# Performance work log

Hardware: AMD Instinct MI355X
Metric: run time of the kernel (lower is better)

Reference implementation:

```python
import jax, jax.numpy as jnp
import numpy as np

WH = WW = 7
SHIFT = 3
H = W = 56
NUM_HEADS = 8
DIM = 256
NW = (H // WH) * (W // WW)  # 64 windows per image
B = 64  # images


def _make_coords_table():
    rch = np.arange(-(WH - 1), WH, dtype=np.float32)
    rcw = np.arange(-(WW - 1), WW, dtype=np.float32)
    t = np.stack(np.meshgrid(rch, rcw, indexing='ij'), axis=-1)[None]  # (1,13,13,2)
    t[..., 0] /= (WH - 1)
    t[..., 1] /= (WW - 1)
    t *= 8.0
    t = np.sign(t) * np.log2(np.abs(t) + 1.0) / np.log2(8.0)
    return t.astype(np.float32)


def _make_rel_pos_index():
    coords = np.stack(np.meshgrid(np.arange(WH), np.arange(WW), indexing='ij'))  # (2,Wh,Ww)
    cf = coords.reshape(2, -1)
    rel = (cf[:, :, None] - cf[:, None, :]).transpose(1, 2, 0)  # (N,N,2)
    rel[..., 0] += WH - 1
    rel[..., 1] += WW - 1
    rel[..., 0] *= 2 * WW - 1
    return rel.sum(-1).astype(np.int32)  # (49,49)


def _make_shift_mask():
    img = np.zeros((H, W), dtype=np.float32)
    cnt = 0
    for hs in (slice(0, -WH), slice(-WH, -SHIFT), slice(-SHIFT, None)):
        for ws in (slice(0, -WW), slice(-WW, -SHIFT), slice(-SHIFT, None)):
            img[hs, ws] = cnt
            cnt += 1
    win = img.reshape(H // WH, WH, W // WW, WW).transpose(0, 2, 1, 3).reshape(-1, WH * WW)
    diff = win[:, None, :] - win[:, :, None]
    return np.where(diff != 0, -100.0, 0.0).astype(np.float32)  # (nW,49,49)


def setup_inputs() -> dict:
    key = jax.random.key(0)
    ks = jax.random.split(key, 10)
    N = WH * WW
    B_ = B * NW
    s = 0.02
    return {
        'x': jax.random.normal(ks[0], (B_, N, DIM), jnp.float32),
        'qkv_w': jax.random.normal(ks[1], (3 * DIM, DIM), jnp.float32) * s,
        'q_bias': jax.random.normal(ks[2], (DIM,), jnp.float32) * s,
        'v_bias': jax.random.normal(ks[3], (DIM,), jnp.float32) * s,
        'logit_scale': jnp.full((NUM_HEADS, 1, 1), np.log(10.0), jnp.float32),
        'cpb_w1': jax.random.normal(ks[4], (512, 2), jnp.float32) * 0.5,
        'cpb_b1': jax.random.normal(ks[5], (512,), jnp.float32) * s,
        'cpb_w2': jax.random.normal(ks[6], (NUM_HEADS, 512), jnp.float32) * 0.05,
        'relative_coords_table': jnp.asarray(_make_coords_table()),
        'relative_position_index': jnp.asarray(_make_rel_pos_index()),
        'attn_mask': jnp.asarray(_make_shift_mask()),
        'proj_w': jax.random.normal(ks[7], (DIM, DIM), jnp.float32) * s,
        'proj_b': jax.random.normal(ks[8], (DIM,), jnp.float32) * s,
    }


def reference(x, qkv_w, q_bias, v_bias, logit_scale, cpb_w1, cpb_b1, cpb_w2,
              relative_coords_table, relative_position_index, attn_mask,
              proj_w, proj_b):
    B_, N, C = x.shape
    nH = logit_scale.shape[0]
    hd = C // nH
    nW = attn_mask.shape[0]
    # qkv projection; k has no bias (SwinV2)
    qkv_bias = jnp.concatenate([q_bias, jnp.zeros_like(v_bias), v_bias])
    qkv = x @ qkv_w.T + qkv_bias
    qkv = qkv.reshape(B_, N, 3, nH, hd).transpose(2, 0, 3, 1, 4)  # (3,B_,nH,N,hd)
    q, k, v = qkv[0], qkv[1], qkv[2]
    # cosine attention (eps matches fused kernel)
    eps = 1e-6
    qn = q * jax.lax.rsqrt(jnp.sum(q * q, axis=-1, keepdims=True) + eps)
    kn = k * jax.lax.rsqrt(jnp.sum(k * k, axis=-1, keepdims=True) + eps)
    attn = jnp.einsum('bhnd,bhmd->bhnm', qn, kn)
    scale = jnp.exp(jnp.minimum(logit_scale, jnp.log(100.0)))  # (nH,1,1), clamp max
    attn = attn * scale[None]
    # continuous relative position bias via CPB MLP
    hcpb = jax.nn.relu(relative_coords_table @ cpb_w1.T + cpb_b1)  # (1,13,13,512)
    table = (hcpb @ cpb_w2.T).reshape(-1, nH)  # (169,nH)
    rpb = table[relative_position_index.reshape(-1)].reshape(N, N, nH).transpose(2, 0, 1)
    rpb = 16.0 * jax.nn.sigmoid(rpb)  # (nH,N,N)
    attn = attn + rpb[None]
    # shift-window mask
    attn = attn.reshape(B_ // nW, nW, nH, N, N) + attn_mask[None, :, None]
    attn = attn.reshape(B_, nH, N, N)
    attn = jax.nn.softmax(attn, axis=-1)
    out = jnp.einsum('bhnm,bhmd->bhnd', attn, v)
    out = out.transpose(0, 2, 1, 3).reshape(B_, N, C)
    return out @ proj_w.T + proj_b
```

## Files before the change

kernel.cpp:

```cpp
#include <hip/hip_runtime.h>
#include <stdint.h>

typedef unsigned short u16;
typedef unsigned int u32;
typedef __attribute__((ext_vector_type(8))) short s16x8;
typedef __attribute__((ext_vector_type(4))) float f32x4;

__device__ __forceinline__ u16 f2bf(float f) {
  union { float f; u32 u; } v; v.f = f;
  u32 u = v.u;
  return (u16)((u + 0x7fffu + ((u >> 16) & 1u)) >> 16);
}
__device__ __forceinline__ float bf2f_lo(u32 u) {
  union { u32 uu; float f; } v; v.uu = u << 16; return v.f;
}
__device__ __forceinline__ float bf2f_hi(u32 u) {
  union { u32 uu; float f; } v; v.uu = u & 0xffff0000u; return v.f;
}
__device__ __forceinline__ void cvt8(uint4 w, float* f) {
  f[0] = bf2f_lo(w.x); f[1] = bf2f_hi(w.x);
  f[2] = bf2f_lo(w.y); f[3] = bf2f_hi(w.y);
  f[4] = bf2f_lo(w.z); f[5] = bf2f_hi(w.z);
  f[6] = bf2f_lo(w.w); f[7] = bf2f_hi(w.w);
}

#define NT 49
#define CD 256
#define NWIN 4096
#define SB_RS 520
#define SX_RS 264
#define SVT_RS 72

#define L_SX  0
#define L_SB  33792
#define L_SVT 100352
#define L_SRQ 137216
#define L_SRK 139264
#define L_TOTAL 141312

#define WS_BIASC 8192
#define WS_WQKV  (8192 + 524288)
#define WS_WPROJ (532480 + 393216)

__global__ void cpb_table_kernel(const float* __restrict__ coords,
                                 const float* __restrict__ w1,
                                 const float* __restrict__ b1,
                                 const float* __restrict__ w2,
                                 float* __restrict__ table) {
  int t = blockIdx.x * 256 + threadIdx.x;
  if (t >= 169 * 8) return;
  int p = t >> 3, h = t & 7;
  float c0 = coords[p * 2], c1 = coords[p * 2 + 1];
  float acc = 0.f;
  for (int j = 0; j < 512; ++j) {
    float hid = fmaf(c0, w1[j * 2], fmaf(c1, w1[j * 2 + 1], b1[j]));
    hid = fmaxf(hid, 0.f);
    acc = fmaf(hid, w2[h * 512 + j], acc);
  }
  table[t] = acc;
}

__global__ void biasc_prep(const float* __restrict__ table,
                           const int* __restrict__ rpi,
                           const float* __restrict__ mask,
                           float* __restrict__ biasC) {
  int idx = blockIdx.x * 256 + threadIdx.x;
  if (idx >= 4 * 8 * 4096) return;
  int t = idx >> 15;
  int h = (idx >> 12) & 7;
  int q = (idx >> 6) & 63;
  int kv = idx & 63;
  float v = -1e9f;
  if (q < 49 && kv < 49) {
    float tb = table[rpi[q * 49 + kv] * 8 + h];
    float rpb = 16.f / (1.f + __expf(-tb));
    int wimg = ((t & 2) ? 56 : 0) + ((t & 1) ? 7 : 0);
    v = rpb + mask[wimg * 2401 + q * 49 + kv];
  }
  biasC[idx] = v;
}

__global__ void wcvt_kernel(const float* __restrict__ qkv_w,
                            const float* __restrict__ proj_w,
                            u16* __restrict__ wq, u16* __restrict__ wp) {
  int t = blockIdx.x * 256 + threadIdx.x;
  if (t >= 32768) return;
  const float* src; u16* dst; int idx;
  if (t < 24576) { idx = t; src = qkv_w; dst = wq + (size_t)idx * 8; }
  else           { idx = t - 24576; src = proj_w; dst = wp + (size_t)idx * 8; }
  int nt = idx >> 9, rem = idx & 511;
  int kk = rem >> 6, l = rem & 63;
  int n = nt * 16 + (l & 15);
  int k = kk * 32 + (l >> 4) * 8;
  const float4* s = (const float4*)(src + (size_t)n * 256 + k);
  float4 v0 = s[0], v1 = s[1];
  u32 w0 = (u32)f2bf(v0.x) | ((u32)f2bf(v0.y) << 16);
  u32 w1 = (u32)f2bf(v0.z) | ((u32)f2bf(v0.w) << 16);
  u32 w2 = (u32)f2bf(v1.x) | ((u32)f2bf(v1.y) << 16);
  u32 w3 = (u32)f2bf(v1.z) | ((u32)f2bf(v1.w) << 16);
  *(uint4*)dst = make_uint4(w0, w1, w2, w3);
}

template<int V0>
__device__ __forceinline__ void p2_body(
    const u16* sX, u16* sB, u16* sVT, const u16* wqb,
    const float* __restrict__ q_bias, const float* __restrict__ v_bias,
    const int hh, const int lr, const int lg) {
  f32x4 acc[6][4];
#pragma unroll
  for (int nt = 0; nt < 6; ++nt)
#pragma unroll
    for (int mt = 0; mt < 4; ++mt) acc[nt][mt] = (f32x4){0.f, 0.f, 0.f, 0.f};
  s16x8 bcur[6], bnxt[6];
#pragma unroll
  for (int nt = 0; nt < 6; ++nt)
    bcur[nt] = *(const s16x8*)&wqb[(nt * 8 + 0) * 512];
#pragma unroll
  for (int kk = 0; kk < 8; ++kk) {
    if (kk < 7) {
#pragma unroll
      for (int nt = 0; nt < 6; ++nt)
        bnxt[nt] = *(const s16x8*)&wqb[(nt * 8 + kk + 1) * 512];
    }
    s16x8 a[4];
#pragma unroll
    for (int mt = 0; mt < 4; ++mt)
      a[mt] = *(const s16x8*)&sX[(mt * 16 + lr) * SX_RS + kk * 32 + lg * 8];
#pragma unroll
    for (int nt = 0; nt < 6; ++nt)
#pragma unroll
      for (int mt = 0; mt < 4; ++mt)
        acc[nt][mt] = (nt < V0)
            ? __builtin_amdgcn_mfma_f32_16x16x32_bf16(bcur[nt], a[mt], acc[nt][mt], 0, 0, 0)
            : __builtin_amdgcn_mfma_f32_16x16x32_bf16(a[mt], bcur[nt], acc[nt][mt], 0, 0, 0);
#pragma unroll
    for (int nt = 0; nt < 6; ++nt) bcur[nt] = bnxt[nt];
  }
#pragma unroll
  for (int nt = 0; nt < 6; ++nt) {
    const int n0 = hh * 96 + nt * 16;
    if (nt < V0) {
      const int r = n0 >> 8;
      const int cb = (n0 & 255) + 4 * lg;
      float4 bq = make_float4(0.f, 0.f, 0.f, 0.f);
      if (r == 0) bq = *(const float4*)(q_bias + cb);
      const int coff = (r << 8) + cb;
#pragma unroll
      for (int mt = 0; mt < 4; ++mt) {
        const int token = mt * 16 + lr;
        if (token < NT) {
          uint2 pk;
          pk.x = (u32)f2bf(acc[nt][mt][0] + bq.x) | ((u32)f2bf(acc[nt][mt][1] + bq.y) << 16);
          pk.y = (u32)f2bf(acc[nt][mt][2] + bq.z) | ((u32)f2bf(acc[nt][mt][3] + bq.w) << 16);
          *(uint2*)&sB[token * SB_RS + coff] = pk;
        }
      }
    } else {
      const int c0 = (n0 & 255) + lr;
      const float bv = v_bias[c0];
      u16* vtb = &sVT[c0 * SVT_RS];
#pragma unroll
      for (int mt = 0; mt < 4; ++mt) {
        const int row0 = mt * 16 + lg * 4;
        float v0 = acc[nt][mt][0] + bv, v1 = acc[nt][mt][1] + bv;
        float v2 = acc[nt][mt][2] + bv, v3 = acc[nt][mt][3] + bv;
        if (mt < 3) {
          uint2 pk2;
          pk2.x = (u32)f2bf(v0) | ((u32)f2bf(v1) << 16);
          pk2.y = (u32)f2bf(v2) | ((u32)f2bf(v3) << 16);
          *(uint2*)&vtb[row0] = pk2;
        } else {
          if (row0     < NT) vtb[row0]     = f2bf(v0);
          if (row0 + 1 < NT) vtb[row0 + 1] = f2bf(v1);
          if (row0 + 2 < NT) vtb[row0 + 2] = f2bf(v2);
          if (row0 + 3 < NT) vtb[row0 + 3] = f2bf(v3);
        }
      }
    }
  }
}

__global__ __launch_bounds__(512, 2) void swin_fused(
    const float* __restrict__ x,
    const float* __restrict__ q_bias, const float* __restrict__ v_bias,
    const float* __restrict__ logit_scale, const float* __restrict__ biasC,
    const u16* __restrict__ wq, const u16* __restrict__ wp,
    const float* __restrict__ proj_b,
    float* __restrict__ out) {
  __shared__ __attribute__((aligned(16))) unsigned char smem[L_TOTAL];
  u16*   sX  = (u16*)(smem + L_SX);
  u16*   sB  = (u16*)(smem + L_SB);
  u16*   sVT = (u16*)(smem + L_SVT);
  float* sRQ = (float*)(smem + L_SRQ);
  float* sRK = (float*)(smem + L_SRK);

  const int tid = threadIdx.x;
  const int wid = blockIdx.x;
  const int wimg = wid & 63;
  const int hh = tid >> 6;
  const int il = tid & 63;
  const int lr = il & 15;
  const int lg = il >> 4;

  float4 xr[6]; float4 xr6;
  {
    const float4* xg = (const float4*)(x + (size_t)wid * (NT * CD));
#pragma unroll
    for (int i = 0; i < 6; ++i) xr[i] = xg[tid + 512 * i];
    if (tid < 64) xr6 = xg[3072 + tid];
  }
  const float scl = __expf(fminf(logit_scale[hh], 4.605170186f));
  {
    u32* zx = (u32*)&sX[49 * SX_RS];
    for (int e = tid; e < 1980; e += 512) zx[e] = 0;
    u32* zb = (u32*)&sB[49 * SB_RS];
    for (int e = tid; e < 3900; e += 512) zb[e] = 0;
    u32* zv = (u32*)sVT;
    for (int e = tid; e < 9216; e += 512) zv[e] = 0;
  }
  {
#pragma unroll
    for (int i = 0; i < 6; ++i) {
      const int e = tid + 512 * i;
      const int row = e >> 6, c4 = e & 63;
      float4 v = xr[i];
      u32 w0 = (u32)f2bf(v.x) | ((u32)f2bf(v.y) << 16);
      u32 w1 = (u32)f2bf(v.z) | ((u32)f2bf(v.w) << 16);
      *(uint2*)&sX[row * SX_RS + c4 * 4] = make_uint2(w0, w1);
    }
    if (tid < 64) {
      const int e = 3072 + tid;
      const int row = e >> 6, c4 = e & 63;
      float4 v = xr6;
      u32 w0 = (u32)f2bf(v.x) | ((u32)f2bf(v.y) << 16);
      u32 w1 = (u32)f2bf(v.z) | ((u32)f2bf(v.w) << 16);
      *(uint2*)&sX[row * SX_RS + c4 * 4] = make_uint2(w0, w1);
    }
  }
  __syncthreads();

  {
    const u16* wqb = wq + (size_t)hh * 24576 + il * 8;
    if (hh < 5)       p2_body<6>(sX, sB, sVT, wqb, q_bias, v_bias, hh, lr, lg);
    else if (hh == 5) p2_body<2>(sX, sB, sVT, wqb, q_bias, v_bias, hh, lr, lg);
    else              p2_body<0>(sX, sB, sVT, wqb, q_bias, v_bias, hh, lr, lg);
  }
  __syncthreads();

  {
    float rqs = 0.f, rkv = 0.f;
    if (il < NT) {
      const uint4* qb4 = (const uint4*)&sB[il * SB_RS + hh * 32];
      const uint4* kb4 = (const uint4*)&sB[il * SB_RS + 256 + hh * 32];
      const int rot = (il >> 3) & 3;
      float f[8];
      float sq = 1e-6f, sk = 1e-6f;
#pragma unroll
      for (int c = 0; c < 4; ++c) {
        const int cg = (c + rot) & 3;
        cvt8(qb4[cg], f);
#pragma unroll
        for (int j = 0; j < 8; ++j) sq = fmaf(f[j], f[j], sq);
      }
#pragma unroll
      for (int c = 0; c < 4; ++c) {
        const int cg = (c + rot) & 3;
        cvt8(kb4[cg], f);
#pragma unroll
        for (int j = 0; j < 8; ++j) sk = fmaf(f[j], f[j], sk);
      }
      rqs = rsqrtf(sq) * scl;
      rkv = rsqrtf(sk);
    }
    sRQ[hh * 64 + il] = rqs;
    sRK[hh * 64 + il] = rkv;
    asm volatile("s_waitcnt lgkmcnt(0)" ::: "memory");
    __builtin_amdgcn_sched_barrier(0);
  }

  {
    const int h = hh;
    const int type = (((wimg >> 3) == 7) ? 2 : 0) | (((wimg & 7) == 7) ? 1 : 0);
    const float* bp = biasC + ((size_t)(type * 8 + h) << 12);
    f32x4 bias[4][4];
#pragma unroll
    for (int nt = 0; nt < 4; ++nt)
#pragma unroll
      for (int mt = 0; mt < 4; ++mt)
        bias[nt][mt] = *(const f32x4*)(bp + (lr + 16 * nt) * 64 + 16 * mt + 4 * lg);
    s16x8 ka[4], qb[4];
#pragma unroll
    for (int mt = 0; mt < 4; ++mt)
      ka[mt] = *(const s16x8*)&sB[(lr + 16 * mt) * SB_RS + 256 + h * 32 + lg * 8];
#pragma unroll
    for (int nt = 0; nt < 4; ++nt)
      qb[nt] = *(const s16x8*)&sB[(lr + 16 * nt) * SB_RS + h * 32 + lg * 8];
    f32x4 sacc[4][4];
#pragma unroll
    for (int nt = 0; nt < 4; ++nt)
#pragma unroll
      for (int mt = 0; mt < 4; ++mt)
        sacc[nt][mt] = __builtin_amdgcn_mfma_f32_16x16x32_bf16(
            ka[mt], qb[nt], (f32x4){0.f, 0.f, 0.f, 0.f}, 0, 0, 0);
    f32x4 rk4[4];
#pragma unroll
    for (int mt = 0; mt < 4; ++mt)
      rk4[mt] = *(const f32x4*)&sRK[h * 64 + 16 * mt + 4 * lg];
    float invv[4];
#pragma unroll
    for (int nt = 0; nt < 4; ++nt) {
      const float rq_ = sRQ[h * 64 + lr + 16 * nt];
      float mx = -3e38f;
#pragma unroll
      for (int mt = 0; mt < 4; ++mt)
#pragma unroll
        for (int i = 0; i < 4; ++i) {
          float tv = fmaf(sacc[nt][mt][i] * rk4[mt][i], rq_, bias[nt][mt][i]);
          sacc[nt][mt][i] = tv;
          mx = fmaxf(mx, tv);
        }
      mx = fmaxf(mx, __shfl_xor(mx, 16, 64));
      mx = fmaxf(mx, __shfl_xor(mx, 32, 64));
      float sm = 0.f;
#pragma unroll
      for (int mt = 0; mt < 4; ++mt)
#pragma unroll
        for (int i = 0; i < 4; ++i) {
          float e = __expf(sacc[nt][mt][i] - mx);
          sacc[nt][mt][i] = e;
          sm += e;
        }
      sm += __shfl_xor(sm, 16, 64);
      sm += __shfl_xor(sm, 32, 64);
      invv[nt] = 1.0f / sm;
    }
    u32 pkk[4][4][2];
#pragma unroll
    for (int nt = 0; nt < 4; ++nt)
#pragma unroll
      for (int mt = 0; mt < 4; ++mt) {
        pkk[nt][mt][0] = (u32)f2bf(sacc[nt][mt][0]) | ((u32)f2bf(sacc[nt][mt][1]) << 16);
        pkk[nt][mt][1] = (u32)f2bf(sacc[nt][mt][2]) | ((u32)f2bf(sacc[nt][mt][3]) << 16);
      }
    s16x8 vb[2][2];
#pragma unroll
    for (int nd = 0; nd < 2; ++nd)
#pragma unroll
      for (int s = 0; s < 2; ++s)
        vb[nd][s] = *(const s16x8*)&sVT[(h * 32 + nd * 16 + lr) * SVT_RS + lg * 8 + 32 * s];
    const int srcA = lr + ((il & 16) << 1);
    const int srcB = srcA + 16;
    const bool gh = (il & 32) != 0;
    f32x4 oacc[4][2];
#pragma unroll
    for (int mo = 0; mo < 4; ++mo)
#pragma unroll
      for (int nd = 0; nd < 2; ++nd) oacc[mo][nd] = (f32x4){0.f, 0.f, 0.f, 0.f};
#pragma unroll
    for (int mo = 0; mo < 4; ++mo) {
#pragma unroll
      for (int s = 0; s < 2; ++s) {
        u32 a0 = (u32)__shfl((int)pkk[mo][2 * s][0],     srcA, 64);
        u32 b0 = (u32)__shfl((int)pkk[mo][2 * s + 1][0], srcA, 64);
        u32 a1 = (u32)__shfl((int)pkk[mo][2 * s][1],     srcA, 64);
        u32 b1 = (u32)__shfl((int)pkk[mo][2 * s + 1][1], srcA, 64);
        u32 a2 = (u32)__shfl((int)pkk[mo][2 * s][0],     srcB, 64);
        u32 b2 = (u32)__shfl((int)pkk[mo][2 * s + 1][0], srcB, 64);
        u32 a3 = (u32)__shfl((int)pkk[mo][2 * s][1],     srcB, 64);
        u32 b3 = (u32)__shfl((int)pkk[mo][2 * s + 1][1], srcB, 64);
        union { u32 u[4]; s16x8 v; } pu;
        pu.u[0] = gh ? b0 : a0;
        pu.u[1] = gh ? b1 : a1;
        pu.u[2] = gh ? b2 : a2;
        pu.u[3] = gh ? b3 : a3;
#pragma unroll
        for (int nd = 0; nd < 2; ++nd)
          oacc[mo][nd] = __builtin_amdgcn_mfma_f32_16x16x32_bf16(
              vb[nd][s], pu.v, oacc[mo][nd], 0, 0, 0);
      }
    }
#pragma unroll
    for (int mo = 0; mo < 4; ++mo) {
      const int q = 16 * mo + lr;
      if (q < NT) {
        const float invq = invv[mo];
#pragma unroll
        for (int nd = 0; nd < 2; ++nd) {
          uint2 pk;
          pk.x = (u32)f2bf(oacc[mo][nd][0] * invq) | ((u32)f2bf(oacc[mo][nd][1] * invq) << 16);
          pk.y = (u32)f2bf(oacc[mo][nd][2] * invq) | ((u32)f2bf(oacc[mo][nd][3] * invq) << 16);
          *(uint2*)&sX[q * SX_RS + h * 32 + nd * 16 + 4 * lg] = pk;
        }
      }
    }
  }
  s16x8 wpr[2][8];
  {
    const u16* wpb = wp + (size_t)hh * 8192 + il * 8;
#pragma unroll
    for (int nt = 0; nt < 2; ++nt)
#pragma unroll
      for (int kk = 0; kk < 8; ++kk)
        wpr[nt][kk] = *(const s16x8*)&wpb[(nt * 8 + kk) * 512];
  }
  float4 pb4[2];
#pragma unroll
  for (int nt = 0; nt < 2; ++nt)
    pb4[nt] = *(const float4*)(proj_b + hh * 32 + nt * 16 + 4 * lg);
  __syncthreads();

  {
    f32x4 acc[2][4];
#pragma unroll
    for (int nt = 0; nt < 2; ++nt)
#pragma unroll
      for (int mt = 0; mt < 4; ++mt) acc[nt][mt] = (f32x4){0.f, 0.f, 0.f, 0.f};
#pragma unroll
    for (int kk = 0; kk < 8; ++kk) {
      s16x8 a[4];
#pragma unroll
      for (int mt = 0; mt < 4; ++mt)
        a[mt] = *(const s16x8*)&sX[(mt * 16 + lr) * SX_RS + kk * 32 + lg * 8];
#pragma unroll
      for (int nt = 0; nt < 2; ++nt)
#pragma unroll
        for (int mt = 0; mt < 4; ++mt)
          acc[nt][mt] = __builtin_amdgcn_mfma_f32_16x16x32_bf16(
              wpr[nt][kk], a[mt], acc[nt][mt], 0, 0, 0);
    }
    float* og = out + (size_t)wid * (NT * CD);
#pragma unroll
    for (int mt = 0; mt < 4; ++mt) {
      const int token = mt * 16 + lr;
      if (token < NT) {
#pragma unroll
        for (int nt = 0; nt < 2; ++nt) {
          float4 st;
          st.x = acc[nt][mt][0] + pb4[nt].x;
          st.y = acc[nt][mt][1] + pb4[nt].y;
          st.z = acc[nt][mt][2] + pb4[nt].z;
          st.w = acc[nt][mt][3] + pb4[nt].w;
          *(float4*)&og[token * CD + hh * 32 + nt * 16 + 4 * lg] = st;
        }
      }
    }
  }
}

extern "C" void kernel_launch(void* const* d_in, const int* in_sizes, int n_in,
                              void* d_out, int out_size, void* d_ws, size_t ws_size,
                              hipStream_t stream) {
  (void)in_sizes; (void)n_in; (void)out_size; (void)ws_size;
  const float* x           = (const float*)d_in[0];
  const float* qkv_w       = (const float*)d_in[1];
  const float* q_bias      = (const float*)d_in[2];
  const float* v_bias      = (const float*)d_in[3];
  const float* logit_scale = (const float*)d_in[4];
  const float* cpb_w1      = (const float*)d_in[5];
  const float* cpb_b1      = (const float*)d_in[6];
  const float* cpb_w2      = (const float*)d_in[7];
  const float* coords      = (const float*)d_in[8];
  const int*   rpi         = (const int*)d_in[9];
  const float* mask        = (const float*)d_in[10];
  const float* proj_w      = (const float*)d_in[11];
  const float* proj_b      = (const float*)d_in[12];
  float* out = (float*)d_out;

  float* table = (float*)d_ws;
  float* biasC = (float*)((char*)d_ws + WS_BIASC);
  u16*   wq    = (u16*)((char*)d_ws + WS_WQKV);
  u16*   wp    = (u16*)((char*)d_ws + WS_WPROJ);

  hipLaunchKernelGGL(cpb_table_kernel, dim3(6), dim3(256), 0, stream,
                     coords, cpb_w1, cpb_b1, cpb_w2, table);
  hipLaunchKernelGGL(biasc_prep, dim3((4 * 8 * 4096 + 255) / 256), dim3(256),
                     0, stream, table, rpi, mask, biasC);
  hipLaunchKernelGGL(wcvt_kernel, dim3(128), dim3(256), 0, stream,
                     qkv_w, proj_w, wq, wp);
  hipLaunchKernelGGL(swin_fused, dim3(NWIN), dim3(512), 0, stream,
                     x, q_bias, v_bias, logit_scale, biasC,
                     wq, wp, proj_b, out);
}
```

Before: 634.7 us.

## Keep per-head Q/K/V in registers, shrink LDS, raise occupancy

Each wave now computes its own head's Q, K and V projections and keeps them in registers. Q/K normalization is done with cross-lane shuffles, and the data is reshaped into MFMA operand layout with shuffles instead of going through shared-memory staging buffers. LDS drops from about 141KB to only the X/output tile, and the launch bound requests 4 blocks per CU instead of 2. The CPB table kernel is also parallelized per position with a wave reduction. The main risk is register pressure at the higher occupancy target and repeated reads of X from LDS across the three projection passes.

```diff
diff --git a/kernel.cpp b/kernel.cpp
--- a/kernel.cpp
+++ b/kernel.cpp
@@ -11,32 +11,14 @@
   u32 u = v.u;
   return (u16)((u + 0x7fffu + ((u >> 16) & 1u)) >> 16);
 }
-__device__ __forceinline__ float bf2f_lo(u32 u) {
-  union { u32 uu; float f; } v; v.uu = u << 16; return v.f;
-}
-__device__ __forceinline__ float bf2f_hi(u32 u) {
-  union { u32 uu; float f; } v; v.uu = u & 0xffff0000u; return v.f;
-}
-__device__ __forceinline__ void cvt8(uint4 w, float* f) {
-  f[0] = bf2f_lo(w.x); f[1] = bf2f_hi(w.x);
-  f[2] = bf2f_lo(w.y); f[3] = bf2f_hi(w.y);
-  f[4] = bf2f_lo(w.z); f[5] = bf2f_hi(w.z);
-  f[6] = bf2f_lo(w.w); f[7] = bf2f_hi(w.w);
+__device__ __forceinline__ u32 pk2bf(float a, float b) {
+  return (u32)f2bf(a) | ((u32)f2bf(b) << 16);
 }
 
 #define NT 49
 #define CD 256
 #define NWIN 4096
-#define SB_RS 520
 #define SX_RS 264
-#define SVT_RS 72
-
-#define L_SX  0
-#define L_SB  33792
-#define L_SVT 100352
-#define L_SRQ 137216
-#define L_SRK 139264
-#define L_TOTAL 141312
 
 #define WS_BIASC 8192
 #define WS_WQKV  (8192 + 524288)
@@ -47,17 +29,29 @@
                                  const float* __restrict__ b1,
                                  const float* __restrict__ w2,
                                  float* __restrict__ table) {
-  int t = blockIdx.x * 256 + threadIdx.x;
-  if (t >= 169 * 8) return;
-  int p = t >> 3, h = t & 7;
-  float c0 = coords[p * 2], c1 = coords[p * 2 + 1];
-  float acc = 0.f;
-  for (int j = 0; j < 512; ++j) {
-    float hid = fmaf(c0, w1[j * 2], fmaf(c1, w1[j * 2 + 1], b1[j]));
-    hid = fmaxf(hid, 0.f);
-    acc = fmaf(hid, w2[h * 512 + j], acc);
-  }
-  table[t] = acc;
+  __shared__ float red[4][8];
+  const int p = blockIdx.x;
+  const int tid = threadIdx.x;
+  const float c0 = coords[p * 2], c1 = coords[p * 2 + 1];
+  float acc[8];
+#pragma unroll
+  for (int h = 0; h < 8; ++h) acc[h] = 0.f;
+  for (int j = tid; j < 512; j += 256) {
+    float hid = fmaxf(fmaf(c0, w1[j * 2], fmaf(c1, w1[j * 2 + 1], b1[j])), 0.f);
+#pragma unroll
+    for (int h = 0; h < 8; ++h) acc[h] = fmaf(hid, w2[h * 512 + j], acc[h]);
+  }
+#pragma unroll
+  for (int h = 0; h < 8; ++h) {
+    float v = acc[h];
+    v += __shfl_xor(v, 1, 64);  v += __shfl_xor(v, 2, 64);
+    v += __shfl_xor(v, 4, 64);  v += __shfl_xor(v, 8, 64);
+    v += __shfl_xor(v, 16, 64); v += __shfl_xor(v, 32, 64);
+    if ((tid & 63) == 0) red[tid >> 6][h] = v;
+  }
+  __syncthreads();
+  if (tid < 8)
+    table[p * 8 + tid] = red[0][tid] + red[1][tid] + red[2][tid] + red[3][tid];
 }
 
 __global__ void biasc_prep(const float* __restrict__ table,
@@ -94,105 +88,31 @@
   int k = kk * 32 + (l >> 4) * 8;
   const float4* s = (const float4*)(src + (size_t)n * 256 + k);
   float4 v0 = s[0], v1 = s[1];
-  u32 w0 = (u32)f2bf(v0.x) | ((u32)f2bf(v0.y) << 16);
-  u32 w1 = (u32)f2bf(v0.z) | ((u32)f2bf(v0.w) << 16);
-  u32 w2 = (u32)f2bf(v1.x) | ((u32)f2bf(v1.y) << 16);
-  u32 w3 = (u32)f2bf(v1.z) | ((u32)f2bf(v1.w) << 16);
-  *(uint4*)dst = make_uint4(w0, w1, w2, w3);
-}
-
-template<int V0>
-__device__ __forceinline__ void p2_body(
-    const u16* sX, u16* sB, u16* sVT, const u16* wqb,
-    const float* __restrict__ q_bias, const float* __restrict__ v_bias,
-    const int hh, const int lr, const int lg) {
-  f32x4 acc[6][4];
-#pragma unroll
-  for (int nt = 0; nt < 6; ++nt)
-#pragma unroll
-    for (int mt = 0; mt < 4; ++mt) acc[nt][mt] = (f32x4){0.f, 0.f, 0.f, 0.f};
-  s16x8 bcur[6], bnxt[6];
-#pragma unroll
-  for (int nt = 0; nt < 6; ++nt)
-    bcur[nt] = *(const s16x8*)&wqb[(nt * 8 + 0) * 512];
-#pragma unroll
-  for (int kk = 0; kk < 8; ++kk) {
-    if (kk < 7) {
-#pragma unroll
-      for (int nt = 0; nt < 6; ++nt)
-        bnxt[nt] = *(const s16x8*)&wqb[(nt * 8 + kk + 1) * 512];
-    }
-    s16x8 a[4];
-#pragma unroll
-    for (int mt = 0; mt < 4; ++mt)
-      a[mt] = *(const s16x8*)&sX[(mt * 16 + lr) * SX_RS + kk * 32 + lg * 8];
-#pragma unroll
-    for (int nt = 0; nt < 6; ++nt)
-#pragma unroll
-      for (int mt = 0; mt < 4; ++mt)
-        acc[nt][mt] = (nt < V0)
-            ? __builtin_amdgcn_mfma_f32_16x16x32_bf16(bcur[nt], a[mt], acc[nt][mt], 0, 0, 0)
-            : __builtin_amdgcn_mfma_f32_16x16x32_bf16(a[mt], bcur[nt], acc[nt][mt], 0, 0, 0);
-#pragma unroll
-    for (int nt = 0; nt < 6; ++nt) bcur[nt] = bnxt[nt];
-  }
-#pragma unroll
-  for (int nt = 0; nt < 6; ++nt) {
-    const int n0 = hh * 96 + nt * 16;
-    if (nt < V0) {
-      const int r = n0 >> 8;
-      const int cb = (n0 & 255) + 4 * lg;
-      float4 bq = make_float4(0.f, 0.f, 0.f, 0.f);
-      if (r == 0) bq = *(const float4*)(q_bias + cb);
-      const int coff = (r << 8) + cb;
-#pragma unroll
-      for (int mt = 0; mt < 4; ++mt) {
-        const int token = mt * 16 + lr;
-        if (token < NT) {
-          uint2 pk;
-          pk.x = (u32)f2bf(acc[nt][mt][0] + bq.x) | ((u32)f2bf(acc[nt][mt][1] + bq.y) << 16);
-          pk.y = (u32)f2bf(acc[nt][mt][2] + bq.z) | ((u32)f2bf(acc[nt][mt][3] + bq.w) << 16);
-          *(uint2*)&sB[token * SB_RS + coff] = pk;
-        }
-      }
-    } else {
-      const int c0 = (n0 & 255) + lr;
-      const float bv = v_bias[c0];
-      u16* vtb = &sVT[c0 * SVT_RS];
-#pragma unroll
-      for (int mt = 0; mt < 4; ++mt) {
-        const int row0 = mt * 16 + lg * 4;
-        float v0 = acc[nt][mt][0] + bv, v1 = acc[nt][mt][1] + bv;
-        float v2 = acc[nt][mt][2] + bv, v3 = acc[nt][mt][3] + bv;
-        if (mt < 3) {
-          uint2 pk2;
-          pk2.x = (u32)f2bf(v0) | ((u32)f2bf(v1) << 16);
-          pk2.y = (u32)f2bf(v2) | ((u32)f2bf(v3) << 16);
-          *(uint2*)&vtb[row0] = pk2;
-        } else {
-          if (row0     < NT) vtb[row0]     = f2bf(v0);
-          if (row0 + 1 < NT) vtb[row0 + 1] = f2bf(v1);
-          if (row0 + 2 < NT) vtb[row0 + 2] = f2bf(v2);
-          if (row0 + 3 < NT) vtb[row0 + 3] = f2bf(v3);
-        }
-      }
-    }
-  }
-}
-
-__global__ __launch_bounds__(512, 2) void swin_fused(
+  *(uint4*)dst = make_uint4(pk2bf(v0.x, v0.y), pk2bf(v0.z, v0.w),
+                            pk2bf(v1.x, v1.y), pk2bf(v1.z, v1.w));
+}
+
+__device__ __forceinline__ s16x8 gather4(const u32 lo0, const u32 lo1,
+                                         const u32 hi0, const u32 hi1,
+                                         int srcL, int srcH, bool hi) {
+  union { u32 u[4]; s16x8 v; } r;
+  u32 a0 = (u32)__shfl((int)lo0, srcL, 64), b0 = (u32)__shfl((int)hi0, srcL, 64);
+  u32 a1 = (u32)__shfl((int)lo1, srcL, 64), b1 = (u32)__shfl((int)hi1, srcL, 64);
+  u32 a2 = (u32)__shfl((int)lo0, srcH, 64), b2 = (u32)__shfl((int)hi0, srcH, 64);
+  u32 a3 = (u32)__shfl((int)lo1, srcH, 64), b3 = (u32)__shfl((int)hi1, srcH, 64);
+  r.u[0] = hi ? b0 : a0; r.u[1] = hi ? b1 : a1;
+  r.u[2] = hi ? b2 : a2; r.u[3] = hi ? b3 : a3;
+  return r.v;
+}
+
+__global__ __launch_bounds__(512, 4) void swin_fused(
     const float* __restrict__ x,
     const float* __restrict__ q_bias, const float* __restrict__ v_bias,
     const float* __restrict__ logit_scale, const float* __restrict__ biasC,
     const u16* __restrict__ wq, const u16* __restrict__ wp,
     const float* __restrict__ proj_b,
     float* __restrict__ out) {
-  __shared__ __attribute__((aligned(16))) unsigned char smem[L_TOTAL];
-  u16*   sX  = (u16*)(smem + L_SX);
-  u16*   sB  = (u16*)(smem + L_SB);
-  u16*   sVT = (u16*)(smem + L_SVT);
-  float* sRQ = (float*)(smem + L_SRQ);
-  float* sRK = (float*)(smem + L_SRK);
+  __shared__ __attribute__((aligned(16))) u16 sX[64 * SX_RS];
 
   const int tid = threadIdx.x;
   const int wid = blockIdx.x;
@@ -201,6 +121,9 @@
   const int il = tid & 63;
   const int lr = il & 15;
   const int lg = il >> 4;
+  const int srcL = lr + 32 * (lg & 1);
+  const int srcH = srcL + 16;
+  const bool hi = (il & 32) != 0;
 
   float4 xr[6]; float4 xr6;
   {
@@ -213,10 +136,6 @@
   {
     u32* zx = (u32*)&sX[49 * SX_RS];
     for (int e = tid; e < 1980; e += 512) zx[e] = 0;
-    u32* zb = (u32*)&sB[49 * SB_RS];
-    for (int e = tid; e < 3900; e += 512) zb[e] = 0;
-    u32* zv = (u32*)sVT;
-    for (int e = tid; e < 9216; e += 512) zv[e] = 0;
   }
   {
 #pragma unroll
@@ -224,101 +143,149 @@
       const int e = tid + 512 * i;
       const int row = e >> 6, c4 = e & 63;
       float4 v = xr[i];
-      u32 w0 = (u32)f2bf(v.x) | ((u32)f2bf(v.y) << 16);
-      u32 w1 = (u32)f2bf(v.z) | ((u32)f2bf(v.w) << 16);
-      *(uint2*)&sX[row * SX_RS + c4 * 4] = make_uint2(w0, w1);
+      *(uint2*)&sX[row * SX_RS + c4 * 4] = make_uint2(pk2bf(v.x, v.y), pk2bf(v.z, v.w));
     }
     if (tid < 64) {
       const int e = 3072 + tid;
       const int row = e >> 6, c4 = e & 63;
       float4 v = xr6;
-      u32 w0 = (u32)f2bf(v.x) | ((u32)f2bf(v.y) << 16);
-      u32 w1 = (u32)f2bf(v.z) | ((u32)f2bf(v.w) << 16);
-      *(uint2*)&sX[row * SX_RS + c4 * 4] = make_uint2(w0, w1);
+      *(uint2*)&sX[row * SX_RS + c4 * 4] = make_uint2(pk2bf(v.x, v.y), pk2bf(v.z, v.w));
     }
   }
   __syncthreads();
 
-  {
-    const u16* wqb = wq + (size_t)hh * 24576 + il * 8;
-    if (hh < 5)       p2_body<6>(sX, sB, sVT, wqb, q_bias, v_bias, hh, lr, lg);
-    else if (hh == 5) p2_body<2>(sX, sB, sVT, wqb, q_bias, v_bias, hh, lr, lg);
-    else              p2_body<0>(sX, sB, sVT, wqb, q_bias, v_bias, hh, lr, lg);
-  }
-  __syncthreads();
-
-  {
-    float rqs = 0.f, rkv = 0.f;
-    if (il < NT) {
-      const uint4* qb4 = (const uint4*)&sB[il * SB_RS + hh * 32];
-      const uint4* kb4 = (const uint4*)&sB[il * SB_RS + 256 + hh * 32];
-      const int rot = (il >> 3) & 3;
-      float f[8];
+  const u16* wqbase = wq + il * 8;
+  s16x8 qbf[4], kaf[4];
+  {
+    f32x4 aq[2][4], ak[2][4];
+#pragma unroll
+    for (int n2 = 0; n2 < 2; ++n2)
+#pragma unroll
+      for (int mt = 0; mt < 4; ++mt) {
+        aq[n2][mt] = (f32x4){0.f, 0.f, 0.f, 0.f};
+        ak[n2][mt] = (f32x4){0.f, 0.f, 0.f, 0.f};
+      }
+    const int nq0 = 2 * hh, nk0 = 16 + 2 * hh;
+#pragma unroll
+    for (int kk = 0; kk < 8; ++kk) {
+      s16x8 a[4];
+#pragma unroll
+      for (int mt = 0; mt < 4; ++mt)
+        a[mt] = *(const s16x8*)&sX[(mt * 16 + lr) * SX_RS + kk * 32 + lg * 8];
+      s16x8 bq0 = *(const s16x8*)&wqbase[((nq0 + 0) * 8 + kk) * 512];
+      s16x8 bq1 = *(const s16x8*)&wqbase[((nq0 + 1) * 8 + kk) * 512];
+      s16x8 bk0 = *(const s16x8*)&wqbase[((nk0 + 0) * 8 + kk) * 512];
+      s16x8 bk1 = *(const s16x8*)&wqbase[((nk0 + 1) * 8 + kk) * 512];
+#pragma unroll
+      for (int mt = 0; mt < 4; ++mt) {
+        aq[0][mt] = __builtin_amdgcn_mfma_f32_16x16x32_bf16(bq0, a[mt], aq[0][mt], 0, 0, 0);
+        aq[1][mt] = __builtin_amdgcn_mfma_f32_16x16x32_bf16(bq1, a[mt], aq[1][mt], 0, 0, 0);
+        ak[0][mt] = __builtin_amdgcn_mfma_f32_16x16x32_bf16(bk0, a[mt], ak[0][mt], 0, 0, 0);
+        ak[1][mt] = __builtin_amdgcn_mfma_f32_16x16x32_bf16(bk1, a[mt], ak[1][mt], 0, 0, 0);
+      }
+    }
+    const float4 qb40 = *(const float4*)(q_bias + 32 * hh + 4 * lg);
+    const float4 qb41 = *(const float4*)(q_bias + 32 * hh + 16 + 4 * lg);
+    float rq[4], rk[4];
+#pragma unroll
+    for (int mt = 0; mt < 4; ++mt) {
+      aq[0][mt][0] += qb40.x; aq[0][mt][1] += qb40.y;
+      aq[0][mt][2] += qb40.z; aq[0][mt][3] += qb40.w;
+      aq[1][mt][0] += qb41.x; aq[1][mt][1] += qb41.y;
+      aq[1][mt][2] += qb41.z; aq[1][mt][3] += qb41.w;
       float sq = 1e-6f, sk = 1e-6f;
 #pragma unroll
-      for (int c = 0; c < 4; ++c) {
-        const int cg = (c + rot) & 3;
-        cvt8(qb4[cg], f);
-#pragma unroll
-        for (int j = 0; j < 8; ++j) sq = fmaf(f[j], f[j], sq);
-      }
-#pragma unroll
-      for (int c = 0; c < 4; ++c) {
-        const int cg = (c + rot) & 3;
-        cvt8(kb4[cg], f);
-#pragma unroll
-        for (int j = 0; j < 8; ++j) sk = fmaf(f[j], f[j], sk);
-      }
-      rqs = rsqrtf(sq) * scl;
-      rkv = rsqrtf(sk);
-    }
-    sRQ[hh * 64 + il] = rqs;
-    sRK[hh * 64 + il] = rkv;
-    asm volatile("s_waitcnt lgkmcnt(0)" ::: "memory");
-    __builtin_amdgcn_sched_barrier(0);
-  }
-
-  {
-    const int h = hh;
+      for (int i = 0; i < 4; ++i) {
+        sq = fmaf(aq[0][mt][i], aq[0][mt][i], sq);
+        sq = fmaf(aq[1][mt][i], aq[1][mt][i], sq);
+        sk = fmaf(ak[0][mt][i], ak[0][mt][i], sk);
+        sk = fmaf(ak[1][mt][i], ak[1][mt][i], sk);
+      }
+      sq += __shfl_xor(sq, 16, 64); sq += __shfl_xor(sq, 32, 64);
+      sk += __shfl_xor(sk, 16, 64); sk += __shfl_xor(sk, 32, 64);
+      rq[mt] = rsqrtf(sq) * scl;
+      rk[mt] = rsqrtf(sk);
+    }
+    u32 pq[2][4][2], pk_[2][4][2];
+#pragma unroll
+    for (int n2 = 0; n2 < 2; ++n2)
+#pragma unroll
+      for (int mt = 0; mt < 4; ++mt) {
+        pq[n2][mt][0] = pk2bf(aq[n2][mt][0] * rq[mt], aq[n2][mt][1] * rq[mt]);
+        pq[n2][mt][1] = pk2bf(aq[n2][mt][2] * rq[mt], aq[n2][mt][3] * rq[mt]);
+        pk_[n2][mt][0] = pk2bf(ak[n2][mt][0] * rk[mt], ak[n2][mt][1] * rk[mt]);
+        pk_[n2][mt][1] = pk2bf(ak[n2][mt][2] * rk[mt], ak[n2][mt][3] * rk[mt]);
+      }
+#pragma unroll
+    for (int nt = 0; nt < 4; ++nt) {
+      qbf[nt] = gather4(pq[0][nt][0], pq[0][nt][1], pq[1][nt][0], pq[1][nt][1], srcL, srcH, hi);
+      kaf[nt] = gather4(pk_[0][nt][0], pk_[0][nt][1], pk_[1][nt][0], pk_[1][nt][1], srcL, srcH, hi);
+    }
+  }
+
+  s16x8 vbf[2][2];
+  {
+    f32x4 av[2][4];
+#pragma unroll
+    for (int n2 = 0; n2 < 2; ++n2)
+#pragma unroll
+      for (int mt = 0; mt < 4; ++mt) av[n2][mt] = (f32x4){0.f, 0.f, 0.f, 0.f};
+    const int nv0 = 32 + 2 * hh;
+#pragma unroll
+    for (int kk = 0; kk < 8; ++kk) {
+      s16x8 a[4];
+#pragma unroll
+      for (int mt = 0; mt < 4; ++mt)
+        a[mt] = *(const s16x8*)&sX[(mt * 16 + lr) * SX_RS + kk * 32 + lg * 8];
+      s16x8 bv0 = *(const s16x8*)&wqbase[((nv0 + 0) * 8 + kk) * 512];
+      s16x8 bv1 = *(const s16x8*)&wqbase[((nv0 + 1) * 8 + kk) * 512];
+#pragma unroll
+      for (int mt = 0; mt < 4; ++mt) {
+        av[0][mt] = __builtin_amdgcn_mfma_f32_16x16x32_bf16(a[mt], bv0, av[0][mt], 0, 0, 0);
+        av[1][mt] = __builtin_amdgcn_mfma_f32_16x16x32_bf16(a[mt], bv1, av[1][mt], 0, 0, 0);
+      }
+    }
+    __syncthreads();
+    const float bv0s = v_bias[32 * hh + lr];
+    const float bv1s = v_bias[32 * hh + 16 + lr];
+    u32 pv[2][4][2];
+#pragma unroll
+    for (int mt = 0; mt < 4; ++mt) {
+      pv[0][mt][0] = pk2bf(av[0][mt][0] + bv0s, av[0][mt][1] + bv0s);
+      pv[0][mt][1] = pk2bf(av[0][mt][2] + bv0s, av[0][mt][3] + bv0s);
+      pv[1][mt][0] = pk2bf(av[1][mt][0] + bv1s, av[1][mt][1] + bv1s);
+      pv[1][mt][1] = pk2bf(av[1][mt][2] + bv1s, av[1][mt][3] + bv1s);
+    }
+#pragma unroll
+    for (int nd = 0; nd < 2; ++nd)
+#pragma unroll
+      for (int s = 0; s < 2; ++s)
+        vbf[nd][s] = gather4(pv[nd][2 * s][0], pv[nd][2 * s][1],
+                             pv[nd][2 * s + 1][0], pv[nd][2 * s + 1][1], srcL, srcH, hi);
+  }
+
+  {
     const int type = (((wimg >> 3) == 7) ? 2 : 0) | (((wimg & 7) == 7) ? 1 : 0);
-    const float* bp = biasC + ((size_t)(type * 8 + h) << 12);
-    f32x4 bias[4][4];
-#pragma unroll
-    for (int nt = 0; nt < 4; ++nt)
-#pragma unroll
-      for (int mt = 0; mt < 4; ++mt)
-        bias[nt][mt] = *(const f32x4*)(bp + (lr + 16 * nt) * 64 + 16 * mt + 4 * lg);
-    s16x8 ka[4], qb[4];
-#pragma unroll
-    for (int mt = 0; mt < 4; ++mt)
-      ka[mt] = *(const s16x8*)&sB[(lr + 16 * mt) * SB_RS + 256 + h * 32 + lg * 8];
-#pragma unroll
-    for (int nt = 0; nt < 4; ++nt)
-      qb[nt] = *(const s16x8*)&sB[(lr + 16 * nt) * SB_RS + h * 32 + lg * 8];
+    const float* bp = biasC + ((size_t)(type * 8 + hh) << 12);
     f32x4 sacc[4][4];
 #pragma unroll
     for (int nt = 0; nt < 4; ++nt)
 #pragma unroll
       for (int mt = 0; mt < 4; ++mt)
         sacc[nt][mt] = __builtin_amdgcn_mfma_f32_16x16x32_bf16(
-            ka[mt], qb[nt], (f32x4){0.f, 0.f, 0.f, 0.f}, 0, 0, 0);
-    f32x4 rk4[4];
-#pragma unroll
-    for (int mt = 0; mt < 4; ++mt)
-      rk4[mt] = *(const f32x4*)&sRK[h * 64 + 16 * mt + 4 * lg];
+            kaf[mt], qbf[nt], (f32x4){0.f, 0.f, 0.f, 0.f}, 0, 0, 0);
     float invv[4];
+    u32 pkk[4][4][2];
 #pragma unroll
     for (int nt = 0; nt < 4; ++nt) {
-      const float rq_ = sRQ[h * 64 + lr + 16 * nt];
       float mx = -3e38f;
 #pragma unroll
-      for (int mt = 0; mt < 4; ++mt)
-#pragma unroll
-        for (int i = 0; i < 4; ++i) {
-          float tv = fmaf(sacc[nt][mt][i] * rk4[mt][i], rq_, bias[nt][mt][i]);
-          sacc[nt][mt][i] = tv;
-          mx = fmaxf(mx, tv);
-        }
+      for (int mt = 0; mt < 4; ++mt) {
+        f32x4 b4 = *(const f32x4*)(bp + (lr + 16 * nt) * 64 + 16 * mt + 4 * lg);
+        sacc[nt][mt] += b4;
+#pragma unroll
+        for (int i = 0; i < 4; ++i) mx = fmaxf(mx, sacc[nt][mt][i]);
+      }
       mx = fmaxf(mx, __shfl_xor(mx, 16, 64));
       mx = fmaxf(mx, __shfl_xor(mx, 32, 64));
       float sm = 0.f;
@@ -333,24 +300,12 @@
       sm += __shfl_xor(sm, 16, 64);
       sm += __shfl_xor(sm, 32, 64);
       invv[nt] = 1.0f / sm;
-    }
-    u32 pkk[4][4][2];
-#pragma unroll
-    for (int nt = 0; nt < 4; ++nt)
-#pragma unroll
-      for (int mt = 0; mt < 4; ++mt) {
-        pkk[nt][mt][0] = (u32)f2bf(sacc[nt][mt][0]) | ((u32)f2bf(sacc[nt][mt][1]) << 16);
-        pkk[nt][mt][1] = (u32)f2bf(sacc[nt][mt][2]) | ((u32)f2bf(sacc[nt][mt][3]) << 16);
-      }
-    s16x8 vb[2][2];
-#pragma unroll
-    for (int nd = 0; nd < 2; ++nd)
-#pragma unroll
-      for (int s = 0; s < 2; ++s)
-        vb[nd][s] = *(const s16x8*)&sVT[(h * 32 + nd * 16 + lr) * SVT_RS + lg * 8 + 32 * s];
-    const int srcA = lr + ((il & 16) << 1);
-    const int srcB = srcA + 16;
-    const bool gh = (il & 32) != 0;
+#pragma unroll
+      for (int mt = 0; mt < 4; ++mt) {
+        pkk[nt][mt][0] = pk2bf(sacc[nt][mt][0], sacc[nt][mt][1]);
+        pkk[nt][mt][1] = pk2bf(sacc[nt][mt][2], sacc[nt][mt][3]);
+      }
+    }
     f32x4 oacc[4][2];
 #pragma unroll
     for (int mo = 0; mo < 4; ++mo)
@@ -360,23 +315,23 @@
     for (int mo = 0; mo < 4; ++mo) {
 #pragma unroll
       for (int s = 0; s < 2; ++s) {
-        u32 a0 = (u32)__shfl((int)pkk[mo][2 * s][0],     srcA, 64);
-        u32 b0 = (u32)__shfl((int)pkk[mo][2 * s + 1][0], srcA, 64);
-        u32 a1 = (u32)__shfl((int)pkk[mo][2 * s][1],     srcA, 64);
-        u32 b1 = (u32)__shfl((int)pkk[mo][2 * s + 1][1], srcA, 64);
-        u32 a2 = (u32)__shfl((int)pkk[mo][2 * s][0],     srcB, 64);
-        u32 b2 = (u32)__shfl((int)pkk[mo][2 * s + 1][0], srcB, 64);
-        u32 a3 = (u32)__shfl((int)pkk[mo][2 * s][1],     srcB, 64);
-        u32 b3 = (u32)__shfl((int)pkk[mo][2 * s + 1][1], srcB, 64);
+        u32 a0 = (u32)__shfl((int)pkk[mo][2 * s][0],     srcL, 64);
+        u32 b0 = (u32)__shfl((int)pkk[mo][2 * s + 1][0], srcL, 64);
+        u32 a1 = (u32)__shfl((int)pkk[mo][2 * s][1],     srcL, 64);
+        u32 b1 = (u32)__shfl((int)pkk[mo][2 * s + 1][1], srcL, 64);
+        u32 a2 = (u32)__shfl((int)pkk[mo][2 * s][0],     srcH, 64);
+        u32 b2 = (u32)__shfl((int)pkk[mo][2 * s + 1][0], srcH, 64);
+        u32 a3 = (u32)__shfl((int)pkk[mo][2 * s][1],     srcH, 64);
+        u32 b3 = (u32)__shfl((int)pkk[mo][2 * s + 1][1], srcH, 64);
         union { u32 u[4]; s16x8 v; } pu;
-        pu.u[0] = gh ? b0 : a0;
-        pu.u[1] = gh ? b1 : a1;
-        pu.u[2] = gh ? b2 : a2;
-        pu.u[3] = gh ? b3 : a3;
+        pu.u[0] = hi ? b0 : a0;
+        pu.u[1] = hi ? b1 : a1;
+        pu.u[2] = hi ? b2 : a2;
+        pu.u[3] = hi ? b3 : a3;
 #pragma unroll
         for (int nd = 0; nd < 2; ++nd)
           oacc[mo][nd] = __builtin_amdgcn_mfma_f32_16x16x32_bf16(
-              vb[nd][s], pu.v, oacc[mo][nd], 0, 0, 0);
+              vbf[nd][s], pu.v, oacc[mo][nd], 0, 0, 0);
       }
     }
 #pragma unroll
@@ -387,29 +342,27 @@
 #pragma unroll
         for (int nd = 0; nd < 2; ++nd) {
           uint2 pk;
-          pk.x = (u32)f2bf(oacc[mo][nd][0] * invq) | ((u32)f2bf(oacc[mo][nd][1] * invq) << 16);
-          pk.y = (u32)f2bf(oacc[mo][nd][2] * invq) | ((u32)f2bf(oacc[mo][nd][3] * invq) << 16);
-          *(uint2*)&sX[q * SX_RS + h * 32 + nd * 16 + 4 * lg] = pk;
+          pk.x = pk2bf(oacc[mo][nd][0] * invq, oacc[mo][nd][1] * invq);
+          pk.y = pk2bf(oacc[mo][nd][2] * invq, oacc[mo][nd][3] * invq);
+          *(uint2*)&sX[q * SX_RS + hh * 32 + nd * 16 + 4 * lg] = pk;
         }
       }
     }
   }
-  s16x8 wpr[2][8];
-  {
+  __syncthreads();
+
+  {
+    s16x8 wpr[2][8];
     const u16* wpb = wp + (size_t)hh * 8192 + il * 8;
 #pragma unroll
     for (int nt = 0; nt < 2; ++nt)
 #pragma unroll
       for (int kk = 0; kk < 8; ++kk)
         wpr[nt][kk] = *(const s16x8*)&wpb[(nt * 8 + kk) * 512];
-  }
-  float4 pb4[2];
-#pragma unroll
-  for (int nt = 0; nt < 2; ++nt)
-    pb4[nt] = *(const float4*)(proj_b + hh * 32 + nt * 16 + 4 * lg);
-  __syncthreads();
-
-  {
+    float4 pb4[2];
+#pragma unroll
+    for (int nt = 0; nt < 2; ++nt)
+      pb4[nt] = *(const float4*)(proj_b + hh * 32 + nt * 16 + 4 * lg);
     f32x4 acc[2][4];
 #pragma unroll
     for (int nt = 0; nt < 2; ++nt)
@@ -471,7 +424,7 @@
   u16*   wq    = (u16*)((char*)d_ws + WS_WQKV);
   u16*   wp    = (u16*)((char*)d_ws + WS_WPROJ);
 
-  hipLaunchKernelGGL(cpb_table_kernel, dim3(6), dim3(256), 0, stream,
+  hipLaunchKernelGGL(cpb_table_kernel, dim3(169), dim3(256), 0, stream,
                      coords, cpb_w1, cpb_b1, cpb_w2, table);
   hipLaunchKernelGGL(biasc_prep, dim3((4 * 8 * 4096 + 255) / 256), dim3(256),
                      0, stream, table, rpi, mask, biasC);
```

Measured after the change: 884.5 us. +39.4%, slower.
